# Optimization experiments

Hardware: AMD Instinct MI355X
Metric: run time of the kernel (lower is better)

## Reference

```python
import jax, jax.numpy as jnp
import numpy as np

B, S, D, E, K = 4, 4096, 2048, 64, 2

def setup_inputs() -> dict:
    key = jax.random.key(0)
    kx, kw = jax.random.split(key)
    x = jax.random.normal(kx, (B, S, D), dtype=jnp.float32)
    W = jax.random.normal(kw, (E, D), dtype=jnp.float32) * (1.0 / np.sqrt(D))
    b = jnp.zeros((E,), dtype=jnp.float32)
    return {"x": x, "W": W, "b": b, "k": K}

def reference(x, W, b, k):
    # logits: [B, S, E]
    logits = jnp.einsum('bsd,ed->bse', x, W) + b
    probs = jax.nn.softmax(logits, axis=-1)
    topk_probs, topk_experts = jax.lax.top_k(probs, k)  # [B,S,k]
    # one-hot over experts, OR-reduce over k -> bool mask [B,S,E]
    onehot = jax.nn.one_hot(topk_experts, E, dtype=jnp.int32)  # [B,S,k,E]
    masks = onehot.sum(axis=-2).astype(jnp.bool_)
    return (masks, probs)
```

## Files before the change

### kernel.cpp

```cpp
#include <hip/hip_runtime.h>
#include <math.h>

#define NTOK    16384
#define DDIM    2048
#define NEXP    64
#define PSTRIDE (NTOK * NEXP)
#define KP      256
#define NPH     8
#define ROWH    264
#define PLANE   (NEXP * ROWH)
#define SLICE   32768

typedef _Float16 half8   __attribute__((ext_vector_type(8)));
typedef _Float16 half4   __attribute__((ext_vector_type(4)));
typedef float    floatx4 __attribute__((ext_vector_type(4)));

__global__ __launch_bounds__(256) void wconv_kernel(
    const float* __restrict__ W, _Float16* __restrict__ ws)
{
    const int idx4 = blockIdx.x * 256 + threadIdx.x;
    const int e    = idx4 >> 9;
    const int kg   = (idx4 & 511) << 2;
    floatx4 w4 = *(const floatx4*)&W[(size_t)e * DDIM + kg];
    half4 h4, l4;
#pragma unroll
    for (int c = 0; c < 4; ++c) {
        float wv = w4[c];
        _Float16 h = (_Float16)wv;
        h4[c] = h;
        l4[c] = (_Float16)((wv - (float)h) * 2048.0f);
    }
    const int p = kg >> 8, kl = kg & 255;
    _Float16* dst = ws + (size_t)p * SLICE + e * 256 + kl;
    *(half4*)dst           = h4;
    *(half4*)(dst + 16384) = l4;
}

__global__ __launch_bounds__(256, 1) void router_kernel(
    const float* __restrict__ x,
    const _Float16* __restrict__ ws,
    const float* __restrict__ bias,
    float* __restrict__ out)
{
    __shared__ _Float16 lds[2][2 * PLANE];

    const int tid  = threadIdx.x;
    const int lane = tid & 63;
    const int wid  = tid >> 6;
    const int t0   = blockIdx.x * 64 + wid * 16;
    const int mrow = lane & 15;
    const int quad = lane >> 4;

    floatx4 acc_hh[4], acc_md[4];
#pragma unroll
    for (int j = 0; j < 4; ++j) { acc_hh[j] = (floatx4)0.0f; acc_md[j] = (floatx4)0.0f; }

    const float* xrow = x + (size_t)(t0 + mrow) * DDIM + quad * 8;

    floatx4 xc[16], xn[16];
    half8   wn[16];

#pragma unroll
    for (int s = 0; s < 8; ++s) {
        xc[2 * s]     = *(const floatx4*)(xrow + s * 32);
        xc[2 * s + 1] = *(const floatx4*)(xrow + s * 32 + 4);
    }
#pragma unroll
    for (int i = 0; i < 16; ++i)
        wn[i] = *(const half8*)(ws + (size_t)(tid + i * 256) * 8);
#pragma unroll
    for (int i = 0; i < 16; ++i) {
        const int c16 = tid + i * 256;
        const int pl  = c16 >> 11, r = c16 & 2047;
        *(half8*)&lds[0][pl * PLANE + (r >> 5) * ROWH + ((r & 31) << 3)] = wn[i];
    }
    __syncthreads();

    const _Float16* lr = &lds[0][0];
    _Float16*       lw = &lds[1][0];

    for (int p = 0; p < NPH; ++p) {
        if (p < NPH - 1) {
            const float* xp = xrow + (p + 1) * KP;
#pragma unroll
            for (int s = 0; s < 8; ++s) {
                xn[2 * s]     = *(const floatx4*)(xp + s * 32);
                xn[2 * s + 1] = *(const floatx4*)(xp + s * 32 + 4);
            }
            const _Float16* wsrc = ws + (size_t)(p + 1) * SLICE;
#pragma unroll
            for (int i = 0; i < 16; ++i)
                wn[i] = *(const half8*)(wsrc + (size_t)(tid + i * 256) * 8);
        }

#pragma unroll
        for (int s = 0; s < 8; ++s) {
            half8 a_hi, a_lo;
#pragma unroll
            for (int i = 0; i < 4; ++i) {
                float fv = xc[2 * s][i];
                _Float16 h = (_Float16)fv;
                a_hi[i] = h;
                a_lo[i] = (_Float16)((fv - (float)h) * 2048.0f);
            }
#pragma unroll
            for (int i = 0; i < 4; ++i) {
                float fv = xc[2 * s + 1][i];
                _Float16 h = (_Float16)fv;
                a_hi[4 + i] = h;
                a_lo[4 + i] = (_Float16)((fv - (float)h) * 2048.0f);
            }
#pragma unroll
            for (int j = 0; j < 4; ++j) {
                const _Float16* bb = lr + (j * 16 + mrow) * ROWH + s * 32 + quad * 8;
                half8 bh = *(const half8*)bb;
                half8 bl = *(const half8*)(bb + PLANE);
                acc_hh[j] = __builtin_amdgcn_mfma_f32_16x16x32_f16(a_hi, bh, acc_hh[j], 0, 0, 0);
                acc_md[j] = __builtin_amdgcn_mfma_f32_16x16x32_f16(a_hi, bl, acc_md[j], 0, 0, 0);
                acc_md[j] = __builtin_amdgcn_mfma_f32_16x16x32_f16(a_lo, bh, acc_md[j], 0, 0, 0);
            }
        }

        if (p < NPH - 1) {
#pragma unroll
            for (int i = 0; i < 16; ++i) {
                const int c16 = tid + i * 256;
                const int pl  = c16 >> 11, r = c16 & 2047;
                *(half8*)&lw[pl * PLANE + (r >> 5) * ROWH + ((r & 31) << 3)] = wn[i];
            }
#pragma unroll
            for (int i = 0; i < 16; ++i) xc[i] = xn[i];
            _Float16* t = (_Float16*)lr; lr = lw; lw = t;
        }
        __syncthreads();
    }

    const int c = mrow;
    float logit[4][4];
#pragma unroll
    for (int j = 0; j < 4; ++j) {
        const float bj = bias[j * 16 + c];
#pragma unroll
        for (int r = 0; r < 4; ++r)
            logit[j][r] = acc_hh[j][r] + acc_md[j][r] * (1.0f / 2048.0f) + bj;
    }

#pragma unroll
    for (int r = 0; r < 4; ++r) {
        const int trow = t0 + quad * 4 + r;

        float m = logit[0][r];
#pragma unroll
        for (int j = 1; j < 4; ++j) m = fmaxf(m, logit[j][r]);
#pragma unroll
        for (int off = 1; off <= 8; off <<= 1) m = fmaxf(m, __shfl_xor(m, off));

        float pj[4], s = 0.0f;
#pragma unroll
        for (int j = 0; j < 4; ++j) { pj[j] = __expf(logit[j][r] - m); s += pj[j]; }
#pragma unroll
        for (int off = 1; off <= 8; off <<= 1) s += __shfl_xor(s, off);
        const float rinv = 1.0f / s;

        float v1 = -1e30f, v2 = -1e30f; int i1 = -1, i2 = -1;
#pragma unroll
        for (int j = 0; j < 4; ++j) {
            float v = logit[j][r]; int e = j * 16 + c;
            if (v > v1 || (v == v1 && e < i1)) { v2 = v1; i2 = i1; v1 = v; i1 = e; }
            else if (v > v2 || (v == v2 && e < i2)) { v2 = v; i2 = e; }
        }
#pragma unroll
        for (int off = 1; off <= 8; off <<= 1) {
            float u1 = __shfl_xor(v1, off); int q1 = __shfl_xor(i1, off);
            float u2 = __shfl_xor(v2, off); int q2 = __shfl_xor(i2, off);
            if (u1 > v1 || (u1 == v1 && q1 < i1)) {
                if (v1 > u2 || (v1 == u2 && i1 < q2)) { v2 = v1; i2 = i1; }
                else                                   { v2 = u2; i2 = q2; }
                v1 = u1; i1 = q1;
            } else {
                if (u1 > v2 || (u1 == v2 && q1 < i2)) { v2 = u1; i2 = q1; }
            }
        }

#pragma unroll
        for (int j = 0; j < 4; ++j) {
            const int col = j * 16 + c;
            const size_t o = (size_t)trow * NEXP + col;
            out[o]           = (col == i1 || col == i2) ? 1.0f : 0.0f;
            out[PSTRIDE + o] = pj[j] * rinv;
        }
    }
}

extern "C" void kernel_launch(void* const* d_in, const int* in_sizes, int n_in,
                              void* d_out, int out_size, void* d_ws, size_t ws_size,
                              hipStream_t stream) {
    const float* x = (const float*)d_in[0];
    const float* W = (const float*)d_in[1];
    const float* b = (const float*)d_in[2];
    (void)in_sizes; (void)n_in; (void)out_size; (void)ws_size;
    float* out = (float*)d_out;

    _Float16* ws = (_Float16*)d_ws;

    hipLaunchKernelGGL(wconv_kernel, dim3(128), dim3(256), 0, stream, W, ws);
    hipLaunchKernelGGL(router_kernel, dim3(NTOK / 64), dim3(256), 0, stream, x, ws, b, out);
}
```

Baseline: 215.6 us.

## Stage weights via direct global-to-LDS loads with XOR swizzle and split-K waves

```diff
diff --git a/kernel.cpp b/kernel.cpp
--- a/kernel.cpp
+++ b/kernel.cpp
@@ -5,49 +5,61 @@
 #define DDIM    2048
 #define NEXP    64
 #define PSTRIDE (NTOK * NEXP)
-#define KP      256
-#define NPH     8
-#define ROWH    264
-#define PLANE   (NEXP * ROWH)
-#define SLICE   32768
+#define KP      128
+#define NPH     16
+#define PLANE_H 8192
+#define SLICE_B 32768
+
+#define AS1 __attribute__((address_space(1)))
+#define AS3 __attribute__((address_space(3)))
 
 typedef _Float16 half8   __attribute__((ext_vector_type(8)));
-typedef _Float16 half4   __attribute__((ext_vector_type(4)));
 typedef float    floatx4 __attribute__((ext_vector_type(4)));
 
 __global__ __launch_bounds__(256) void wconv_kernel(
     const float* __restrict__ W, _Float16* __restrict__ ws)
 {
-    const int idx4 = blockIdx.x * 256 + threadIdx.x;
-    const int e    = idx4 >> 9;
-    const int kg   = (idx4 & 511) << 2;
-    floatx4 w4 = *(const floatx4*)&W[(size_t)e * DDIM + kg];
-    half4 h4, l4;
-#pragma unroll
-    for (int c = 0; c < 4; ++c) {
-        float wv = w4[c];
-        _Float16 h = (_Float16)wv;
-        h4[c] = h;
-        l4[c] = (_Float16)((wv - (float)h) * 2048.0f);
-    }
-    const int p = kg >> 8, kl = kg & 255;
-    _Float16* dst = ws + (size_t)p * SLICE + e * 256 + kl;
-    *(half4*)dst           = h4;
-    *(half4*)(dst + 16384) = l4;
+    const int g     = blockIdx.x * 256 + threadIdx.x;
+    const int p     = g >> 11;
+    const int L     = g & 2047;
+    const int plane = L >> 10;
+    const int e     = (L >> 4) & 63;
+    const int cp    = L & 15;
+    const int c     = cp ^ (e & 7);
+    const int k     = (p << 7) + (c << 3);
+
+    const float* src = &W[(size_t)e * DDIM + k];
+    floatx4 w0 = *(const floatx4*)src;
+    floatx4 w1 = *(const floatx4*)(src + 4);
+
+    half8 o;
+#pragma unroll
+    for (int i = 0; i < 4; ++i) {
+        float f0 = w0[i], f1 = w1[i];
+        _Float16 h0 = (_Float16)f0, h1 = (_Float16)f1;
+        if (plane == 0) { o[i] = h0; o[4 + i] = h1; }
+        else {
+            o[i]     = (_Float16)((f0 - (float)h0) * 2048.0f);
+            o[4 + i] = (_Float16)((f1 - (float)h1) * 2048.0f);
+        }
+    }
+    *(half8*)((char*)ws + (size_t)g * 16) = o;
 }
 
-__global__ __launch_bounds__(256, 1) void router_kernel(
+__global__ __launch_bounds__(256, 2) void router_kernel(
     const float* __restrict__ x,
     const _Float16* __restrict__ ws,
     const float* __restrict__ bias,
     float* __restrict__ out)
 {
-    __shared__ _Float16 lds[2][2 * PLANE];
+    __shared__ _Float16 lds[2][SLICE_B / 2];
 
     const int tid  = threadIdx.x;
     const int lane = tid & 63;
     const int wid  = tid >> 6;
-    const int t0   = blockIdx.x * 64 + wid * 16;
+    const int t    = wid >> 1;
+    const int h    = wid & 1;
+    const int t0   = blockIdx.x * 32 + t * 16;
     const int mrow = lane & 15;
     const int quad = lane >> 4;
 
@@ -55,66 +67,70 @@
 #pragma unroll
     for (int j = 0; j < 4; ++j) { acc_hh[j] = (floatx4)0.0f; acc_md[j] = (floatx4)0.0f; }
 
-    const float* xrow = x + (size_t)(t0 + mrow) * DDIM + quad * 8;
-
-    floatx4 xc[16], xn[16];
-    half8   wn[16];
-
-#pragma unroll
-    for (int s = 0; s < 8; ++s) {
+    const float* xrow = x + (size_t)(t0 + mrow) * DDIM + h * 64 + quad * 8;
+
+    const char* gslice0 = (const char*)ws;
+    char*       lbase[2] = { (char*)&lds[0][0] + wid * 8192,
+                             (char*)&lds[1][0] + wid * 8192 };
+
+#define STAGE(P, BUF)                                                          \
+    {                                                                          \
+        const char* gsrc = gslice0 + (size_t)(P) * SLICE_B + wid * 8192 + lane * 16; \
+        char*       ldst = lbase[BUF];                                         \
+        _Pragma("unroll")                                                      \
+        for (int i = 0; i < 8; ++i)                                            \
+            __builtin_amdgcn_global_load_lds(                                  \
+                (const AS1 unsigned int*)(const void*)(gsrc + i * 1024),       \
+                (AS3 unsigned int*)(void*)(ldst + i * 1024), 16, 0, 0);        \
+    }
+
+    floatx4 xc[4], xn[4];
+
+    STAGE(0, 0);
+#pragma unroll
+    for (int s = 0; s < 2; ++s) {
         xc[2 * s]     = *(const floatx4*)(xrow + s * 32);
         xc[2 * s + 1] = *(const floatx4*)(xrow + s * 32 + 4);
     }
-#pragma unroll
-    for (int i = 0; i < 16; ++i)
-        wn[i] = *(const half8*)(ws + (size_t)(tid + i * 256) * 8);
-#pragma unroll
-    for (int i = 0; i < 16; ++i) {
-        const int c16 = tid + i * 256;
-        const int pl  = c16 >> 11, r = c16 & 2047;
-        *(half8*)&lds[0][pl * PLANE + (r >> 5) * ROWH + ((r & 31) << 3)] = wn[i];
-    }
     __syncthreads();
 
-    const _Float16* lr = &lds[0][0];
-    _Float16*       lw = &lds[1][0];
-
+#pragma unroll 2
     for (int p = 0; p < NPH; ++p) {
         if (p < NPH - 1) {
+            STAGE(p + 1, (p + 1) & 1);
             const float* xp = xrow + (p + 1) * KP;
 #pragma unroll
-            for (int s = 0; s < 8; ++s) {
+            for (int s = 0; s < 2; ++s) {
                 xn[2 * s]     = *(const floatx4*)(xp + s * 32);
                 xn[2 * s + 1] = *(const floatx4*)(xp + s * 32 + 4);
             }
-            const _Float16* wsrc = ws + (size_t)(p + 1) * SLICE;
-#pragma unroll
-            for (int i = 0; i < 16; ++i)
-                wn[i] = *(const half8*)(wsrc + (size_t)(tid + i * 256) * 8);
-        }
-
-#pragma unroll
-        for (int s = 0; s < 8; ++s) {
+        }
+
+        const _Float16* lb = &lds[p & 1][0];
+#pragma unroll
+        for (int s = 0; s < 2; ++s) {
             half8 a_hi, a_lo;
 #pragma unroll
             for (int i = 0; i < 4; ++i) {
                 float fv = xc[2 * s][i];
-                _Float16 h = (_Float16)fv;
-                a_hi[i] = h;
-                a_lo[i] = (_Float16)((fv - (float)h) * 2048.0f);
+                _Float16 hh = (_Float16)fv;
+                a_hi[i] = hh;
+                a_lo[i] = (_Float16)((fv - (float)hh) * 2048.0f);
             }
 #pragma unroll
             for (int i = 0; i < 4; ++i) {
                 float fv = xc[2 * s + 1][i];
-                _Float16 h = (_Float16)fv;
-                a_hi[4 + i] = h;
-                a_lo[4 + i] = (_Float16)((fv - (float)h) * 2048.0f);
+                _Float16 hh = (_Float16)fv;
+                a_hi[4 + i] = hh;
+                a_lo[4 + i] = (_Float16)((fv - (float)hh) * 2048.0f);
             }
 #pragma unroll
             for (int j = 0; j < 4; ++j) {
-                const _Float16* bb = lr + (j * 16 + mrow) * ROWH + s * 32 + quad * 8;
-                half8 bh = *(const half8*)bb;
-                half8 bl = *(const half8*)(bb + PLANE);
+                const int e   = j * 16 + mrow;
+                const int c   = h * 8 + s * 4 + quad;
+                const int off = e * 128 + ((c ^ (e & 7)) << 3);
+                half8 bh = *(const half8*)(lb + off);
+                half8 bl = *(const half8*)(lb + PLANE_H + off);
                 acc_hh[j] = __builtin_amdgcn_mfma_f32_16x16x32_f16(a_hi, bh, acc_hh[j], 0, 0, 0);
                 acc_md[j] = __builtin_amdgcn_mfma_f32_16x16x32_f16(a_hi, bl, acc_md[j], 0, 0, 0);
                 acc_md[j] = __builtin_amdgcn_mfma_f32_16x16x32_f16(a_lo, bh, acc_md[j], 0, 0, 0);
@@ -123,41 +139,51 @@
 
         if (p < NPH - 1) {
 #pragma unroll
-            for (int i = 0; i < 16; ++i) {
-                const int c16 = tid + i * 256;
-                const int pl  = c16 >> 11, r = c16 & 2047;
-                *(half8*)&lw[pl * PLANE + (r >> 5) * ROWH + ((r & 31) << 3)] = wn[i];
-            }
-#pragma unroll
-            for (int i = 0; i < 16; ++i) xc[i] = xn[i];
-            _Float16* t = (_Float16*)lr; lr = lw; lw = t;
+            for (int i = 0; i < 4; ++i) xc[i] = xn[i];
         }
         __syncthreads();
     }
 
+    float lg[4][4];
+#pragma unroll
+    for (int j = 0; j < 4; ++j)
+#pragma unroll
+        for (int r = 0; r < 4; ++r)
+            lg[j][r] = acc_hh[j][r] + acc_md[j][r] * (1.0f / 2048.0f);
+
+    float* rbuf = (float*)&lds[0][0];
+    if (h == 1) {
+#pragma unroll
+        for (int j = 0; j < 4; ++j)
+#pragma unroll
+            for (int r = 0; r < 4; ++r)
+                rbuf[t * 1024 + (j * 4 + r) * 64 + lane] = lg[j][r];
+    }
+    __syncthreads();
+    if (h == 1) return;
+
+#pragma unroll
+    for (int j = 0; j < 4; ++j) {
+        const float bj = bias[j * 16 + mrow];
+#pragma unroll
+        for (int r = 0; r < 4; ++r)
+            lg[j][r] += rbuf[t * 1024 + (j * 4 + r) * 64 + lane] + bj;
+    }
+
     const int c = mrow;
-    float logit[4][4];
-#pragma unroll
-    for (int j = 0; j < 4; ++j) {
-        const float bj = bias[j * 16 + c];
-#pragma unroll
-        for (int r = 0; r < 4; ++r)
-            logit[j][r] = acc_hh[j][r] + acc_md[j][r] * (1.0f / 2048.0f) + bj;
-    }
-
 #pragma unroll
     for (int r = 0; r < 4; ++r) {
         const int trow = t0 + quad * 4 + r;
 
-        float m = logit[0][r];
-#pragma unroll
-        for (int j = 1; j < 4; ++j) m = fmaxf(m, logit[j][r]);
+        float m = lg[0][r];
+#pragma unroll
+        for (int j = 1; j < 4; ++j) m = fmaxf(m, lg[j][r]);
 #pragma unroll
         for (int off = 1; off <= 8; off <<= 1) m = fmaxf(m, __shfl_xor(m, off));
 
         float pj[4], s = 0.0f;
 #pragma unroll
-        for (int j = 0; j < 4; ++j) { pj[j] = __expf(logit[j][r] - m); s += pj[j]; }
+        for (int j = 0; j < 4; ++j) { pj[j] = __expf(lg[j][r] - m); s += pj[j]; }
 #pragma unroll
         for (int off = 1; off <= 8; off <<= 1) s += __shfl_xor(s, off);
         const float rinv = 1.0f / s;
@@ -165,7 +191,7 @@
         float v1 = -1e30f, v2 = -1e30f; int i1 = -1, i2 = -1;
 #pragma unroll
         for (int j = 0; j < 4; ++j) {
-            float v = logit[j][r]; int e = j * 16 + c;
+            float v = lg[j][r]; int e = j * 16 + c;
             if (v > v1 || (v == v1 && e < i1)) { v2 = v1; i2 = i1; v1 = v; i1 = e; }
             else if (v > v2 || (v == v2 && e < i2)) { v2 = v; i2 = e; }
         }
@@ -204,5 +230,5 @@
     _Float16* ws = (_Float16*)d_ws;
 
     hipLaunchKernelGGL(wconv_kernel, dim3(128), dim3(256), 0, stream, W, ws);
-    hipLaunchKernelGGL(router_kernel, dim3(NTOK / 64), dim3(256), 0, stream, x, ws, b, out);
+    hipLaunchKernelGGL(router_kernel, dim3(NTOK / 32), dim3(256), 0, stream, x, ws, b, out);
 }
```

New measurement: 200.3 us. -7.1%, faster.
